# Kernel optimization log

Measured on AMD Instinct MI355X. Metric: run time of the kernel, lower is better.

Reference implementation:

```python
import jax, jax.numpy as jnp
import numpy as np

N_NODES = 50000
N_EDGES = 800000
D_IN = 128
D_GAT = 128
D_LIN = 512
D_OUT = 4
N_CONVS = 3


def setup_inputs() -> dict:
    key = jax.random.key(0)
    ks = jax.random.split(key, 16)
    s = 1.0 / np.sqrt(D_GAT)
    inp = {
        "x": jax.random.normal(ks[0], (N_NODES, D_IN), dtype=jnp.float32),
        "edge_index": jax.random.randint(ks[1], (2, N_EDGES), 0, N_NODES, dtype=jnp.int64),
        # 3 GATConv layers (input_dim == hidden_gat_dim so params stack)
        "conv_W": jax.random.normal(ks[2], (N_CONVS, D_GAT, D_GAT), dtype=jnp.float32) * s,
        "conv_a_src": jax.random.normal(ks[3], (N_CONVS, D_GAT), dtype=jnp.float32) * s,
        "conv_a_dst": jax.random.normal(ks[4], (N_CONVS, D_GAT), dtype=jnp.float32) * s,
        "conv_b": jnp.zeros((N_CONVS, D_GAT), dtype=jnp.float32),
        # MLP head: 128->512, 512->512, 512->512, 512->4
        "lin_W0": jax.random.normal(ks[5], (D_GAT, D_LIN), dtype=jnp.float32) / np.sqrt(D_GAT),
        "lin_b0": jnp.zeros((D_LIN,), dtype=jnp.float32),
        "lin_W1": jax.random.normal(ks[6], (D_LIN, D_LIN), dtype=jnp.float32) / np.sqrt(D_LIN),
        "lin_b1": jnp.zeros((D_LIN,), dtype=jnp.float32),
        "lin_W2": jax.random.normal(ks[7], (D_LIN, D_LIN), dtype=jnp.float32) / np.sqrt(D_LIN),
        "lin_b2": jnp.zeros((D_LIN,), dtype=jnp.float32),
        "lin_Wout": jax.random.normal(ks[8], (D_LIN, D_OUT), dtype=jnp.float32) / np.sqrt(D_LIN),
        "lin_bout": jnp.zeros((D_OUT,), dtype=jnp.float32),
    }
    return inp


def _gat_layer(x, src, dst, W, a_src, a_dst, b, n):
    """PyG-style single-head GATConv with self loops already in (src, dst)."""
    h = x @ W                                    # [N, F]
    e = (h @ a_src)[src] + (h @ a_dst)[dst]      # per-edge raw score [E]
    e = jax.nn.leaky_relu(e, 0.2)
    # segment softmax over destination node neighborhoods
    m = jax.ops.segment_max(e, dst, num_segments=n)
    ex = jnp.exp(e - m[dst])
    denom = jax.ops.segment_sum(ex, dst, num_segments=n)
    alpha = ex / denom[dst]                      # [E]
    out = jax.ops.segment_sum(alpha[:, None] * h[src], dst, num_segments=n)
    return out + b


def reference(x, edge_index, conv_W, conv_a_src, conv_a_dst, conv_b,
              lin_W0, lin_b0, lin_W1, lin_b1, lin_W2, lin_b2, lin_Wout, lin_bout):
    n = x.shape[0]
    loops = jnp.arange(n, dtype=edge_index.dtype)
    src = jnp.concatenate([edge_index[0], loops])  # add self loops (PyG default)
    dst = jnp.concatenate([edge_index[1], loops])
    for i in range(N_CONVS):
        x = _gat_layer(x, src, dst, conv_W[i], conv_a_src[i], conv_a_dst[i], conv_b[i], n)
        x = jax.nn.leaky_relu(x, 0.2)
    for W, b in ((lin_W0, lin_b0), (lin_W1, lin_b1), (lin_W2, lin_b2)):
        x = jax.nn.relu(x @ W + b)  # F.relu(x, 0.2): 0.2 is truthy inplace flag -> plain relu
    return x @ lin_Wout + lin_bout
```

## Files before the change

### kernel.cpp

```cpp
#include <hip/hip_runtime.h>
#include <hip/hip_bf16.h>

#define NN 50000
#define NE 800000
#define NET (NE + NN)
#define SCAN_NB ((NN + 255) / 256)

static inline int imin(int a, int b) { return a < b ? a : b; }

typedef _Float16 half8 __attribute__((ext_vector_type(8)));
typedef _Float16 half2v __attribute__((ext_vector_type(2)));
typedef float f32x4 __attribute__((ext_vector_type(4)));

__global__ void k_count(const int* __restrict__ edst, int* __restrict__ counts) {
    int e = blockIdx.x * blockDim.x + threadIdx.x;
    if (e >= NET) return;
    int d = (e < NE) ? edst[e] : (e - NE);
    atomicAdd(&counts[d], 1);
}

__global__ __launch_bounds__(256) void k_scan1(const int* __restrict__ counts,
                                               int* __restrict__ part) {
    __shared__ int s[256];
    int t = threadIdx.x, i = blockIdx.x * 256 + t;
    s[t] = (i < NN) ? counts[i] : 0;
    __syncthreads();
    for (int off = 128; off > 0; off >>= 1) {
        if (t < off) s[t] += s[t + off];
        __syncthreads();
    }
    if (t == 0) part[blockIdx.x] = s[0];
}

__global__ __launch_bounds__(256) void k_scan2(int* __restrict__ part, int* __restrict__ offs) {
    __shared__ int s[256];
    int t = threadIdx.x;
    int v = (t < SCAN_NB) ? part[t] : 0;
    s[t] = v;
    __syncthreads();
    for (int off = 1; off < 256; off <<= 1) {
        int a = (t >= off) ? s[t - off] : 0;
        __syncthreads();
        s[t] += a;
        __syncthreads();
    }
    if (t < SCAN_NB) part[t] = s[t] - v;
    if (t == 255) offs[NN] = s[255];
}

__global__ __launch_bounds__(256) void k_scan3(const int* __restrict__ counts,
                                               const int* __restrict__ part,
                                               int* __restrict__ offs, int* __restrict__ cursor) {
    __shared__ int s[256];
    int t = threadIdx.x, i = blockIdx.x * 256 + t;
    int v = (i < NN) ? counts[i] : 0;
    s[t] = v;
    __syncthreads();
    for (int off = 1; off < 256; off <<= 1) {
        int a = (t >= off) ? s[t - off] : 0;
        __syncthreads();
        s[t] += a;
        __syncthreads();
    }
    if (i < NN) {
        int e = part[blockIdx.x] + s[t] - v;
        offs[i] = e;
        cursor[i] = e;
    }
}

__global__ void k_scatter(const int* __restrict__ esrc, const int* __restrict__ edst,
                          int* __restrict__ cursor, int* __restrict__ csr_src) {
    int e = blockIdx.x * blockDim.x + threadIdx.x;
    if (e >= NET) return;
    int s, d;
    if (e < NE) { s = esrc[e]; d = edst[e]; } else { s = e - NE; d = s; }
    int pos = atomicAdd(&cursor[d], 1);
    csr_src[pos] = s;
}

__global__ void k_split(const float* __restrict__ in, _Float16* __restrict__ hi,
                        _Float16* __restrict__ lo, int n) {
    int i = blockIdx.x * blockDim.x + threadIdx.x;
    int st = gridDim.x * blockDim.x;
    for (; i < n; i += st) {
        float v = in[i];
        _Float16 h = (_Float16)v;
        hi[i] = h;
        lo[i] = (_Float16)(v - (float)h);
    }
}

__global__ __launch_bounds__(256) void k_prepw(const float* __restrict__ W,
                                               _Float16* __restrict__ Th,
                                               _Float16* __restrict__ Tl, int K, int N) {
    __shared__ float tile[32][33];
    int tx = threadIdx.x & 31, ty = threadIdx.x >> 5;
    int n0 = blockIdx.x * 32, k0 = blockIdx.y * 32;
    #pragma unroll
    for (int r = ty; r < 32; r += 8)
        tile[r][tx] = W[(size_t)(k0 + r) * N + n0 + tx];
    __syncthreads();
    #pragma unroll
    for (int r = ty; r < 32; r += 8) {
        int n = n0 + r, k = k0 + tx;
        float v = tile[tx][r];
        _Float16 h = (_Float16)v;
        Th[(size_t)n * K + k] = h;
        Tl[(size_t)n * K + k] = (_Float16)(v - (float)h);
    }
}

__global__ void k_aggregate(const _Float16* __restrict__ h, const float* __restrict__ s_src,
                            const float* __restrict__ s_dst, const int* __restrict__ offs,
                            const int* __restrict__ csr_src, const float* __restrict__ bias,
                            _Float16* __restrict__ xh, _Float16* __restrict__ xl) {
    int node = blockIdx.x * 4 + (threadIdx.x >> 6);
    int lane = threadIdx.x & 63;
    if (node >= NN) return;
    int p = offs[node], pe = offs[node + 1];
    float sd = s_dst[node];
    float den = 0.f, acc0 = 0.f, acc1 = 0.f;
    for (; p + 4 <= pe; p += 4) {
        int s0 = csr_src[p + 0], s1 = csr_src[p + 1];
        int s2 = csr_src[p + 2], s3 = csr_src[p + 3];
        float e0 = s_src[s0] + sd, e1 = s_src[s1] + sd;
        float e2 = s_src[s2] + sd, e3 = s_src[s3] + sd;
        half2v a0 = *((const half2v*)(h + (size_t)s0 * 128) + lane);
        half2v a1 = *((const half2v*)(h + (size_t)s1 * 128) + lane);
        half2v a2 = *((const half2v*)(h + (size_t)s2 * 128) + lane);
        half2v a3 = *((const half2v*)(h + (size_t)s3 * 128) + lane);
        e0 = (e0 > 0.f) ? e0 : 0.2f * e0;  float w0 = __expf(e0);
        e1 = (e1 > 0.f) ? e1 : 0.2f * e1;  float w1 = __expf(e1);
        e2 = (e2 > 0.f) ? e2 : 0.2f * e2;  float w2 = __expf(e2);
        e3 = (e3 > 0.f) ? e3 : 0.2f * e3;  float w3 = __expf(e3);
        den += (w0 + w1) + (w2 + w3);
        acc0 += w0 * (float)a0[0] + w1 * (float)a1[0] + w2 * (float)a2[0] + w3 * (float)a3[0];
        acc1 += w0 * (float)a0[1] + w1 * (float)a1[1] + w2 * (float)a2[1] + w3 * (float)a3[1];
    }
    for (; p < pe; ++p) {
        int src = csr_src[p];
        float e = s_src[src] + sd;
        e = (e > 0.f) ? e : 0.2f * e;
        float wgt = __expf(e);
        den += wgt;
        half2v av = *((const half2v*)(h + (size_t)src * 128) + lane);
        acc0 += wgt * (float)av[0];
        acc1 += wgt * (float)av[1];
    }
    float inv = 1.f / den;
    float2 bv = *((const float2*)bias + lane);
    float v0 = acc0 * inv + bv.x;
    float v1 = acc1 * inv + bv.y;
    v0 = (v0 > 0.f) ? v0 : 0.2f * v0;
    v1 = (v1 > 0.f) ? v1 : 0.2f * v1;
    _Float16 h0 = (_Float16)v0, h1 = (_Float16)v1;
    size_t base = (size_t)node * 128 + 2 * lane;
    *(half2v*)(xh + base) = (half2v){h0, h1};
    *(half2v*)(xl + base) = (half2v){(_Float16)(v0 - (float)h0), (_Float16)(v1 - (float)h1)};
}

__device__ __forceinline__ void gload_lds16(const void* g, void* l) {
    __builtin_amdgcn_global_load_lds(
        (const __attribute__((address_space(1))) void*)g,
        (__attribute__((address_space(3))) void*)l, 16, 0, 0);
}

__device__ __forceinline__ void phase_stagger(int bid) {
    int ph = (int)(((unsigned)bid * 2654435761u) >> 29);
    for (int i = 0; i < ph; ++i) __builtin_amdgcn_s_sleep(8);
}

__global__ __launch_bounds__(512) void k_mgemm(
    const _Float16* __restrict__ Ahi, const _Float16* __restrict__ Alo,
    const _Float16* __restrict__ Bhi, const _Float16* __restrict__ Blo,
    const float* __restrict__ bias, float* __restrict__ Cf,
    _Float16* __restrict__ Chi, _Float16* __restrict__ Clo,
    int M, int N, int K, int relu, int split, int nx, int ntiles)
{
    __shared__ _Float16 sm[4][128][32];

    int bid = blockIdx.x;
    int per = (ntiles + 7) >> 3;
    int g = (bid & 7) * per + (bid >> 3);
    if (g >= ntiles) return;
    int col0 = (g % nx) * 128;
    int row0 = (g / nx) * 128;

    phase_stagger(bid);

    int t = threadIdx.x;
    int w = t >> 6, lane = t & 63;
    int wm = (w & 3) * 32, wn = (w >> 2) * 64;
    int fr = lane & 15;
    int fq = lane >> 4, fq8 = fq * 8;

    int srow = t >> 2;
    int scol = (t & 3) << 3;
    int lrow = w << 4;

    f32x4 acc[2][4];
    #pragma unroll
    for (int i = 0; i < 2; i++)
        #pragma unroll
        for (int j = 0; j < 4; j++) acc[i][j] = (f32x4){0.f, 0.f, 0.f, 0.f};

    for (int k0 = 0; k0 < K; k0 += 32) {
        if (k0) __syncthreads();
        {
            int ga = row0 + srow; if (ga > M - 1) ga = M - 1;
            int gb = col0 + srow;
            gload_lds16(Ahi + (size_t)ga * K + k0 + scol, &sm[0][lrow][0]);
            gload_lds16(Alo + (size_t)ga * K + k0 + scol, &sm[1][lrow][0]);
            gload_lds16(Bhi + (size_t)gb * K + k0 + scol, &sm[2][lrow][0]);
            gload_lds16(Blo + (size_t)gb * K + k0 + scol, &sm[3][lrow][0]);
        }
        __syncthreads();

        half8 bh[4], bl[4];
        #pragma unroll
        for (int ni = 0; ni < 4; ++ni) {
            bh[ni] = *(half8*)&sm[2][wn + ni * 16 + fr][fq8];
            bl[ni] = *(half8*)&sm[3][wn + ni * 16 + fr][fq8];
        }
        #pragma unroll
        for (int mi = 0; mi < 2; ++mi) {
            half8 ah = *(half8*)&sm[0][wm + mi * 16 + fr][fq8];
            half8 al = *(half8*)&sm[1][wm + mi * 16 + fr][fq8];
            #pragma unroll
            for (int ni = 0; ni < 4; ++ni) {
                acc[mi][ni] = __builtin_amdgcn_mfma_f32_16x16x32_f16(ah, bh[ni], acc[mi][ni], 0, 0, 0);
                acc[mi][ni] = __builtin_amdgcn_mfma_f32_16x16x32_f16(ah, bl[ni], acc[mi][ni], 0, 0, 0);
                acc[mi][ni] = __builtin_amdgcn_mfma_f32_16x16x32_f16(al, bh[ni], acc[mi][ni], 0, 0, 0);
            }
        }
    }

    float bv[4];
    #pragma unroll
    for (int ni = 0; ni < 4; ++ni)
        bv[ni] = bias ? bias[col0 + wn + ni * 16 + fr] : 0.f;

    if (split) {
        _Float16* sc = &sm[0][0][0];
        #pragma unroll
        for (int pass = 0; pass < 2; ++pass) {
            __syncthreads();
            #pragma unroll
            for (int mi = 0; mi < 2; ++mi) {
                #pragma unroll
                for (int ni = 0; ni < 4; ++ni) {
                    #pragma unroll
                    for (int r = 0; r < 4; ++r) {
                        int row = wm + mi * 16 + fq * 4 + r;
                        int col = wn + ni * 16 + fr;
                        float v = acc[mi][ni][r] + bv[ni];
                        if (relu) v = (v > 0.f) ? v : 0.f;
                        _Float16 hh = (_Float16)v;
                        sc[row * 128 + col] = pass ? (_Float16)(v - (float)hh) : hh;
                    }
                }
            }
            __syncthreads();
            _Float16* dst = pass ? Clo : Chi;
            #pragma unroll
            for (int pp = 0; pp < 4; ++pp) {
                int idx = t + pp * 512;
                int row = idx >> 4, seg = idx & 15;
                int gr = row0 + row;
                if (gr < M)
                    *(half8*)(dst + (size_t)gr * N + col0 + seg * 8) =
                        *(half8*)&sc[row * 128 + seg * 8];
            }
        }
    } else {
        #pragma unroll
        for (int ni = 0; ni < 4; ++ni) {
            #pragma unroll
            for (int mi = 0; mi < 2; ++mi) {
                #pragma unroll
                for (int r = 0; r < 4; ++r) {
                    int gr = row0 + wm + mi * 16 + fq * 4 + r;
                    if (gr >= M) continue;
                    float v = acc[mi][ni][r] + bv[ni];
                    if (relu) v = (v > 0.f) ? v : 0.f;
                    Cf[(size_t)gr * N + col0 + wn + ni * 16 + fr] = v;
                }
            }
        }
    }
}

__global__ __launch_bounds__(256) void k_mgemm_gat(
    const _Float16* __restrict__ Ahi, const _Float16* __restrict__ Alo,
    const _Float16* __restrict__ Bhi, const _Float16* __restrict__ Blo,
    const float* __restrict__ a_src, const float* __restrict__ a_dst,
    _Float16* __restrict__ hbuf, float* __restrict__ s_src, float* __restrict__ s_dst,
    int M, int ntiles)
{
    __shared__ _Float16 sm[4][128][32];
    __shared__ float sps[2][128], spd[2][128];

    const int K = 128;
    int bid = blockIdx.x;
    int per = (ntiles + 7) >> 3;
    int g = (bid & 7) * per + (bid >> 3);
    if (g >= ntiles) return;
    int row0 = g * 128;

    int t = threadIdx.x;
    int w = t >> 6, lane = t & 63;
    int wm = (w & 1) * 64, wn = (w >> 1) * 64;
    int fr = lane & 15;
    int fq = lane >> 4, fq8 = fq * 8;
    int wnIdx = w >> 1;

    int srow = (w << 5) + (lane >> 2);
    int scol = (lane & 3) << 3;

    f32x4 acc[4][4];
    #pragma unroll
    for (int i = 0; i < 4; i++)
        #pragma unroll
        for (int j = 0; j < 4; j++) acc[i][j] = (f32x4){0.f, 0.f, 0.f, 0.f};

    for (int k0 = 0; k0 < K; k0 += 32) {
        if (k0) __syncthreads();
        #pragma unroll
        for (int i = 0; i < 2; ++i) {
            int rr = srow + i * 16;
            int ga = row0 + rr; if (ga > M - 1) ga = M - 1;
            int gb = rr;
            int lr = (w << 5) + i * 16;
            gload_lds16(Ahi + (size_t)ga * K + k0 + scol, &sm[0][lr][0]);
            gload_lds16(Alo + (size_t)ga * K + k0 + scol, &sm[1][lr][0]);
            gload_lds16(Bhi + (size_t)gb * K + k0 + scol, &sm[2][lr][0]);
            gload_lds16(Blo + (size_t)gb * K + k0 + scol, &sm[3][lr][0]);
        }
        __syncthreads();

        half8 bh[4], bl[4];
        #pragma unroll
        for (int ni = 0; ni < 4; ++ni) {
            bh[ni] = *(half8*)&sm[2][wn + ni * 16 + fr][fq8];
            bl[ni] = *(half8*)&sm[3][wn + ni * 16 + fr][fq8];
        }
        #pragma unroll
        for (int mi = 0; mi < 4; ++mi) {
            half8 ah = *(half8*)&sm[0][wm + mi * 16 + fr][fq8];
            half8 al = *(half8*)&sm[1][wm + mi * 16 + fr][fq8];
            #pragma unroll
            for (int ni = 0; ni < 4; ++ni) {
                acc[mi][ni] = __builtin_amdgcn_mfma_f32_16x16x32_f16(ah, bh[ni], acc[mi][ni], 0, 0, 0);
                acc[mi][ni] = __builtin_amdgcn_mfma_f32_16x16x32_f16(ah, bl[ni], acc[mi][ni], 0, 0, 0);
                acc[mi][ni] = __builtin_amdgcn_mfma_f32_16x16x32_f16(al, bh[ni], acc[mi][ni], 0, 0, 0);
            }
        }
    }

    float asv[4], adv[4];
    #pragma unroll
    for (int ni = 0; ni < 4; ++ni) {
        int gc = wn + ni * 16 + fr;
        asv[ni] = a_src[gc];
        adv[ni] = a_dst[gc];
    }
    #pragma unroll
    for (int mi = 0; mi < 4; ++mi) {
        #pragma unroll
        for (int r = 0; r < 4; ++r) {
            int lr = wm + mi * 16 + fq * 4 + r;
            int gr = row0 + lr;
            float vps = 0.f, vpd = 0.f;
            #pragma unroll
            for (int ni = 0; ni < 4; ++ni) {
                float v = acc[mi][ni][r];
                vps += v * asv[ni];
                vpd += v * adv[ni];
                if (gr < M) hbuf[(size_t)gr * 128 + wn + ni * 16 + fr] = (_Float16)v;
            }
            #pragma unroll
            for (int off = 1; off < 16; off <<= 1) {
                vps += __shfl_xor(vps, off);
                vpd += __shfl_xor(vpd, off);
            }
            if (fr == 0) { sps[wnIdx][lr] = vps; spd[wnIdx][lr] = vpd; }
        }
    }
    __syncthreads();
    if (t < 128) {
        int gr = row0 + t;
        if (gr < M) {
            s_src[gr] = sps[0][t] + sps[1][t];
            s_dst[gr] = spd[0][t] + spd[1][t];
        }
    }
}

__global__ __launch_bounds__(256) void k_mgemm_head(
    const _Float16* __restrict__ Ahi, const _Float16* __restrict__ Alo,
    const _Float16* __restrict__ Bhi, const _Float16* __restrict__ Blo,
    const float* __restrict__ bias, const float* __restrict__ Wo,
    float* __restrict__ partial,
    int M, int K, int nx, int ntiles)
{
    __shared__ _Float16 sm[4][128][32];
    __shared__ float4 sacc[2][128];

    int bid = blockIdx.x;
    int per = (ntiles + 7) >> 3;
    int g = (bid & 7) * per + (bid >> 3);
    if (g >= ntiles) return;
    int ct = g % nx;
    int col0 = ct * 128;
    int row0 = (g / nx) * 128;

    phase_stagger(bid);

    int t = threadIdx.x;
    int w = t >> 6, lane = t & 63;
    int wm = (w & 1) * 64, wn = (w >> 1) * 64;
    int fr = lane & 15;
    int fq = lane >> 4, fq8 = fq * 8;

    int srow = (w << 5) + (lane >> 2);
    int scol = (lane & 3) << 3;

    f32x4 acc[4][4];
    #pragma unroll
    for (int i = 0; i < 4; i++)
        #pragma unroll
        for (int j = 0; j < 4; j++) acc[i][j] = (f32x4){0.f, 0.f, 0.f, 0.f};

    for (int k0 = 0; k0 < K; k0 += 32) {
        if (k0) __syncthreads();
        #pragma unroll
        for (int i = 0; i < 2; ++i) {
            int rr = srow + i * 16;
            int ga = row0 + rr; if (ga > M - 1) ga = M - 1;
            int gb = col0 + rr;
            int lr = (w << 5) + i * 16;
            gload_lds16(Ahi + (size_t)ga * K + k0 + scol, &sm[0][lr][0]);
            gload_lds16(Alo + (size_t)ga * K + k0 + scol, &sm[1][lr][0]);
            gload_lds16(Bhi + (size_t)gb * K + k0 + scol, &sm[2][lr][0]);
            gload_lds16(Blo + (size_t)gb * K + k0 + scol, &sm[3][lr][0]);
        }
        __syncthreads();

        half8 bh[4], bl[4];
        #pragma unroll
        for (int ni = 0; ni < 4; ++ni) {
            bh[ni] = *(half8*)&sm[2][wn + ni * 16 + fr][fq8];
            bl[ni] = *(half8*)&sm[3][wn + ni * 16 + fr][fq8];
        }
        #pragma unroll
        for (int mi = 0; mi < 4; ++mi) {
            half8 ah = *(half8*)&sm[0][wm + mi * 16 + fr][fq8];
            half8 al = *(half8*)&sm[1][wm + mi * 16 + fr][fq8];
            #pragma unroll
            for (int ni = 0; ni < 4; ++ni) {
                acc[mi][ni] = __builtin_amdgcn_mfma_f32_16x16x32_f16(ah, bh[ni], acc[mi][ni], 0, 0, 0);
                acc[mi][ni] = __builtin_amdgcn_mfma_f32_16x16x32_f16(ah, bl[ni], acc[mi][ni], 0, 0, 0);
                acc[mi][ni] = __builtin_amdgcn_mfma_f32_16x16x32_f16(al, bh[ni], acc[mi][ni], 0, 0, 0);
            }
        }
    }

    float bv[4];
    float4 wv[4];
    #pragma unroll
    for (int ni = 0; ni < 4; ++ni) {
        int gc = col0 + wn + ni * 16 + fr;
        bv[ni] = bias[gc];
        wv[ni] = *(const float4*)(Wo + (size_t)gc * 4);
    }
    #pragma unroll
    for (int mi = 0; mi < 4; ++mi) {
        #pragma unroll
        for (int r = 0; r < 4; ++r) {
            int lr = wm + mi * 16 + fq * 4 + r;
            float o0 = 0.f, o1 = 0.f, o2 = 0.f, o3 = 0.f;
            #pragma unroll
            for (int ni = 0; ni < 4; ++ni) {
                float v = acc[mi][ni][r] + bv[ni];
                v = (v > 0.f) ? v : 0.f;
                o0 += v * wv[ni].x; o1 += v * wv[ni].y;
                o2 += v * wv[ni].z; o3 += v * wv[ni].w;
            }
            #pragma unroll
            for (int off = 1; off < 16; off <<= 1) {
                o0 += __shfl_xor(o0, off); o1 += __shfl_xor(o1, off);
                o2 += __shfl_xor(o2, off); o3 += __shfl_xor(o3, off);
            }
            if (fr == 0) sacc[w >> 1][lr] = (float4){o0, o1, o2, o3};
        }
    }
    __syncthreads();
    if (t < 128) {
        int gr = row0 + t;
        if (gr < M) {
            float4 s0 = sacc[0][t], s1 = sacc[1][t];
            float4 o = (float4){s0.x + s1.x, s0.y + s1.y, s0.z + s1.z, s0.w + s1.w};
            *(float4*)(partial + ((size_t)ct * M + gr) * 4) = o;
        }
    }
}

__global__ __launch_bounds__(256) void k_headred(const float* __restrict__ partial,
                                                 const float* __restrict__ bo,
                                                 float* __restrict__ out, int M) {
    int r = blockIdx.x * 256 + threadIdx.x;
    if (r >= M) return;
    float4 a = *(const float4*)(partial + ((size_t)0 * M + r) * 4);
    float4 b = *(const float4*)(partial + ((size_t)1 * M + r) * 4);
    float4 c = *(const float4*)(partial + ((size_t)2 * M + r) * 4);
    float4 d = *(const float4*)(partial + ((size_t)3 * M + r) * 4);
    float4 o;
    o.x = a.x + b.x + c.x + d.x + bo[0];
    o.y = a.y + b.y + c.y + d.y + bo[1];
    o.z = a.z + b.z + c.z + d.z + bo[2];
    o.w = a.w + b.w + c.w + d.w + bo[3];
    *(float4*)(out + (size_t)r * 4) = o;
}

extern "C" void kernel_launch(void* const* d_in, const int* in_sizes, int n_in,
                              void* d_out, int out_size, void* d_ws, size_t ws_size,
                              hipStream_t stream) {
    const float* x    = (const float*)d_in[0];
    const int*   eidx = (const int*)d_in[1];
    const float* cW   = (const float*)d_in[2];
    const float* caS  = (const float*)d_in[3];
    const float* caD  = (const float*)d_in[4];
    const float* cB   = (const float*)d_in[5];
    const float* W0   = (const float*)d_in[6];
    const float* b0   = (const float*)d_in[7];
    const float* W1   = (const float*)d_in[8];
    const float* b1   = (const float*)d_in[9];
    const float* W2   = (const float*)d_in[10];
    const float* b2   = (const float*)d_in[11];
    const float* Wo   = (const float*)d_in[12];
    const float* bo   = (const float*)d_in[13];
    (void)in_sizes; (void)n_in; (void)out_size;

    const int* esrc = eidx;
    const int* edst = eidx + NE;
    float* out = (float*)d_out;

    char* w = (char*)d_ws;
    auto alloc = [&](size_t bytes) -> char* {
        char* p = w;
        w += (bytes + 255) & ~(size_t)255;
        return p;
    };
    _Float16* x0h  = (_Float16*)alloc((size_t)NN * 128 * 2);
    _Float16* x0l  = (_Float16*)alloc((size_t)NN * 128 * 2);
    _Float16* xh   = (_Float16*)alloc((size_t)NN * 128 * 2);
    _Float16* xl   = (_Float16*)alloc((size_t)NN * 128 * 2);
    _Float16* hbuf = (_Float16*)alloc((size_t)NN * 128 * 2);
    float* ssrc    = (float*)alloc((size_t)NN * 4);
    float* sdst    = (float*)alloc((size_t)NN * 4);
    int*   counts  = (int*)  alloc((size_t)NN * 4);
    int*   offs    = (int*)  alloc((size_t)(NN + 1) * 4);
    int*   cursor  = (int*)  alloc((size_t)NN * 4);
    int*   csr     = (int*)  alloc((size_t)NET * 4);
    int*   part    = (int*)  alloc((size_t)SCAN_NB * 4);
    _Float16* cwh  = (_Float16*)alloc(3 * 128 * 128 * 2);
    _Float16* cwl  = (_Float16*)alloc(3 * 128 * 128 * 2);
    _Float16* w0h  = (_Float16*)alloc(512 * 128 * 2);
    _Float16* w0l  = (_Float16*)alloc(512 * 128 * 2);
    _Float16* w1h  = (_Float16*)alloc(512 * 512 * 2);
    _Float16* w1l  = (_Float16*)alloc(512 * 512 * 2);
    _Float16* w2h  = (_Float16*)alloc(512 * 512 * 2);
    _Float16* w2l  = (_Float16*)alloc(512 * 512 * 2);
    float* hpart   = (float*)alloc((size_t)4 * NN * 4 * 4);

    size_t used = (size_t)(w - (char*)d_ws);
    size_t rem = (ws_size > used) ? (ws_size - used) : 0;
    int chunk = (int)(rem / (4 * 512 * sizeof(_Float16)));
    if (chunk > NN) chunk = NN;
    if (chunk > 128) chunk &= ~127;
    if (chunk < 1) chunk = 1;
    _Float16* Y0h = (_Float16*)alloc((size_t)chunk * 512 * 2);
    _Float16* Y0l = (_Float16*)alloc((size_t)chunk * 512 * 2);
    _Float16* Y1h = (_Float16*)alloc((size_t)chunk * 512 * 2);
    _Float16* Y1l = (_Float16*)alloc((size_t)chunk * 512 * 2);

    auto gemm = [&](const _Float16* Ah, const _Float16* Al,
                    const _Float16* Bh, const _Float16* Bl,
                    const float* bias, float* Cf, _Float16* Ch, _Float16* Cl,
                    int M, int N, int K, int relu, int split) {
        int nx = N / 128;
        int ntiles = nx * ((M + 127) / 128);
        int nb = ((ntiles + 7) / 8) * 8;
        k_mgemm<<<nb, 512, 0, stream>>>(Ah, Al, Bh, Bl, bias, Cf, Ch, Cl,
                                        M, N, K, relu, split, nx, ntiles);
    };

    k_split<<<2048, 256, 0, stream>>>(x, x0h, x0l, NN * 128);
    for (int L = 0; L < 3; ++L)
        k_prepw<<<dim3(128 / 32, 128 / 32), 256, 0, stream>>>(
            cW + (size_t)L * 128 * 128, cwh + (size_t)L * 128 * 128, cwl + (size_t)L * 128 * 128, 128, 128);
    k_prepw<<<dim3(512 / 32, 128 / 32), 256, 0, stream>>>(W0, w0h, w0l, 128, 512);
    k_prepw<<<dim3(512 / 32, 512 / 32), 256, 0, stream>>>(W1, w1h, w1l, 512, 512);
    k_prepw<<<dim3(512 / 32, 512 / 32), 256, 0, stream>>>(W2, w2h, w2l, 512, 512);

    hipMemsetAsync(counts, 0, (size_t)NN * 4, stream);
    int eblocks = (NET + 255) / 256;
    k_count <<<eblocks, 256, 0, stream>>>(edst, counts);
    k_scan1 <<<SCAN_NB, 256, 0, stream>>>(counts, part);
    k_scan2 <<<1, 256, 0, stream>>>(part, offs);
    k_scan3 <<<SCAN_NB, 256, 0, stream>>>(counts, part, offs, cursor);
    k_scatter<<<eblocks, 256, 0, stream>>>(esrc, edst, cursor, csr);

    int gat_tiles = (NN + 127) / 128;
    int gat_nb = ((gat_tiles + 7) / 8) * 8;
    for (int L = 0; L < 3; ++L) {
        const _Float16* Ah = (L == 0) ? x0h : xh;
        const _Float16* Al = (L == 0) ? x0l : xl;
        k_mgemm_gat<<<gat_nb, 256, 0, stream>>>(
            Ah, Al, cwh + (size_t)L * 128 * 128, cwl + (size_t)L * 128 * 128,
            caS + L * 128, caD + L * 128, hbuf, ssrc, sdst, NN, gat_tiles);
        k_aggregate<<<NN / 4, 256, 0, stream>>>(hbuf, ssrc, sdst, offs, csr, cB + L * 128, xh, xl);
    }

    for (int m0 = 0; m0 < NN; m0 += chunk) {
        int cm = imin(chunk, NN - m0);
        gemm(xh + (size_t)m0 * 128, xl + (size_t)m0 * 128, w0h, w0l, b0,
             nullptr, Y0h, Y0l, cm, 512, 128, 1, 1);
        gemm(Y0h, Y0l, w1h, w1l, b1, nullptr, Y1h, Y1l, cm, 512, 512, 1, 1);
        int nx = 4;
        int ntiles = nx * ((cm + 127) / 128);
        int nb = ((ntiles + 7) / 8) * 8;
        k_mgemm_head<<<nb, 256, 0, stream>>>(Y1h, Y1l, w2h, w2l, b2, Wo,
                                             hpart, cm, 512, nx, ntiles);
        k_headred<<<(cm + 255) / 256, 256, 0, stream>>>(hpart, bo, out + (size_t)m0 * 4, cm);
    }
}
```

Measured before the change: 649.6 us.

## Use 512-thread blocks with 8 waves in GAT and head GEMMs, stage hbuf via LDS

Doubles the block size of the GAT projection and head GEMM kernels from 4 to 8 waves. Each wave now computes a 32x64 sub-tile instead of 64x64, which halves the accumulator registers per wave and means each thread issues one set of global-to-LDS loads per K step instead of two. The GAT kernel also writes its fp16 output tile to shared memory first and then copies it to global memory with coalesced 16-byte row stores. The trade-off is more waves sharing the same tile with less MFMA work each, and one extra barrier plus an LDS round trip in the epilogue.

```diff
diff --git a/kernel.cpp b/kernel.cpp
--- a/kernel.cpp
+++ b/kernel.cpp
@@ -291,7 +291,7 @@
     }
 }
 
-__global__ __launch_bounds__(256) void k_mgemm_gat(
+__global__ __launch_bounds__(512) void k_mgemm_gat(
     const _Float16* __restrict__ Ahi, const _Float16* __restrict__ Alo,
     const _Float16* __restrict__ Bhi, const _Float16* __restrict__ Blo,
     const float* __restrict__ a_src, const float* __restrict__ a_dst,
@@ -310,32 +310,30 @@
 
     int t = threadIdx.x;
     int w = t >> 6, lane = t & 63;
-    int wm = (w & 1) * 64, wn = (w >> 1) * 64;
+    int wm = (w & 3) * 32, wn = (w >> 2) * 64;
     int fr = lane & 15;
     int fq = lane >> 4, fq8 = fq * 8;
-    int wnIdx = w >> 1;
-
-    int srow = (w << 5) + (lane >> 2);
-    int scol = (lane & 3) << 3;
-
-    f32x4 acc[4][4];
-    #pragma unroll
-    for (int i = 0; i < 4; i++)
+    int wnIdx = w >> 2;
+
+    int srow = t >> 2;
+    int scol = (t & 3) << 3;
+    int lrow = w << 4;
+
+    f32x4 acc[2][4];
+    #pragma unroll
+    for (int i = 0; i < 2; i++)
         #pragma unroll
         for (int j = 0; j < 4; j++) acc[i][j] = (f32x4){0.f, 0.f, 0.f, 0.f};
 
     for (int k0 = 0; k0 < K; k0 += 32) {
         if (k0) __syncthreads();
-        #pragma unroll
-        for (int i = 0; i < 2; ++i) {
-            int rr = srow + i * 16;
-            int ga = row0 + rr; if (ga > M - 1) ga = M - 1;
-            int gb = rr;
-            int lr = (w << 5) + i * 16;
-            gload_lds16(Ahi + (size_t)ga * K + k0 + scol, &sm[0][lr][0]);
-            gload_lds16(Alo + (size_t)ga * K + k0 + scol, &sm[1][lr][0]);
-            gload_lds16(Bhi + (size_t)gb * K + k0 + scol, &sm[2][lr][0]);
-            gload_lds16(Blo + (size_t)gb * K + k0 + scol, &sm[3][lr][0]);
+        {
+            int ga = row0 + srow; if (ga > M - 1) ga = M - 1;
+            int gb = srow;
+            gload_lds16(Ahi + (size_t)ga * K + k0 + scol, &sm[0][lrow][0]);
+            gload_lds16(Alo + (size_t)ga * K + k0 + scol, &sm[1][lrow][0]);
+            gload_lds16(Bhi + (size_t)gb * K + k0 + scol, &sm[2][lrow][0]);
+            gload_lds16(Blo + (size_t)gb * K + k0 + scol, &sm[3][lrow][0]);
         }
         __syncthreads();
 
@@ -346,7 +344,7 @@
             bl[ni] = *(half8*)&sm[3][wn + ni * 16 + fr][fq8];
         }
         #pragma unroll
-        for (int mi = 0; mi < 4; ++mi) {
+        for (int mi = 0; mi < 2; ++mi) {
             half8 ah = *(half8*)&sm[0][wm + mi * 16 + fr][fq8];
             half8 al = *(half8*)&sm[1][wm + mi * 16 + fr][fq8];
             #pragma unroll
@@ -365,26 +363,27 @@
         asv[ni] = a_src[gc];
         adv[ni] = a_dst[gc];
     }
-    #pragma unroll
-    for (int mi = 0; mi < 4; ++mi) {
+    __syncthreads();
+    _Float16* sc = &sm[0][0][0];
+    #pragma unroll
+    for (int mi = 0; mi < 2; ++mi) {
         #pragma unroll
         for (int r = 0; r < 4; ++r) {
-            int lr = wm + mi * 16 + fq * 4 + r;
-            int gr = row0 + lr;
+            int row = wm + mi * 16 + fq * 4 + r;
             float vps = 0.f, vpd = 0.f;
             #pragma unroll
             for (int ni = 0; ni < 4; ++ni) {
                 float v = acc[mi][ni][r];
                 vps += v * asv[ni];
                 vpd += v * adv[ni];
-                if (gr < M) hbuf[(size_t)gr * 128 + wn + ni * 16 + fr] = (_Float16)v;
+                sc[row * 128 + wn + ni * 16 + fr] = (_Float16)v;
             }
             #pragma unroll
             for (int off = 1; off < 16; off <<= 1) {
                 vps += __shfl_xor(vps, off);
                 vpd += __shfl_xor(vpd, off);
             }
-            if (fr == 0) { sps[wnIdx][lr] = vps; spd[wnIdx][lr] = vpd; }
+            if (fr == 0) { sps[wnIdx][row] = vps; spd[wnIdx][row] = vpd; }
         }
     }
     __syncthreads();
@@ -395,9 +394,17 @@
             s_dst[gr] = spd[0][t] + spd[1][t];
         }
     }
-}
-
-__global__ __launch_bounds__(256) void k_mgemm_head(
+    #pragma unroll
+    for (int pp = 0; pp < 4; ++pp) {
+        int idx = t + pp * 512;
+        int row = idx >> 4, seg = idx & 15;
+        int gr = row0 + row;
+        if (gr < M)
+            *(half8*)(hbuf + (size_t)gr * 128 + seg * 8) = *(half8*)&sc[row * 128 + seg * 8];
+    }
+}
+
+__global__ __launch_bounds__(512) void k_mgemm_head(
     const _Float16* __restrict__ Ahi, const _Float16* __restrict__ Alo,
     const _Float16* __restrict__ Bhi, const _Float16* __restrict__ Blo,
     const float* __restrict__ bias, const float* __restrict__ Wo,
@@ -419,31 +426,29 @@
 
     int t = threadIdx.x;
     int w = t >> 6, lane = t & 63;
-    int wm = (w & 1) * 64, wn = (w >> 1) * 64;
+    int wm = (w & 3) * 32, wn = (w >> 2) * 64;
     int fr = lane & 15;
     int fq = lane >> 4, fq8 = fq * 8;
 
-    int srow = (w << 5) + (lane >> 2);
-    int scol = (lane & 3) << 3;
-
-    f32x4 acc[4][4];
-    #pragma unroll
-    for (int i = 0; i < 4; i++)
+    int srow = t >> 2;
+    int scol = (t & 3) << 3;
+    int lrow = w << 4;
+
+    f32x4 acc[2][4];
+    #pragma unroll
+    for (int i = 0; i < 2; i++)
         #pragma unroll
         for (int j = 0; j < 4; j++) acc[i][j] = (f32x4){0.f, 0.f, 0.f, 0.f};
 
     for (int k0 = 0; k0 < K; k0 += 32) {
         if (k0) __syncthreads();
-        #pragma unroll
-        for (int i = 0; i < 2; ++i) {
-            int rr = srow + i * 16;
-            int ga = row0 + rr; if (ga > M - 1) ga = M - 1;
-            int gb = col0 + rr;
-            int lr = (w << 5) + i * 16;
-            gload_lds16(Ahi + (size_t)ga * K + k0 + scol, &sm[0][lr][0]);
-            gload_lds16(Alo + (size_t)ga * K + k0 + scol, &sm[1][lr][0]);
-            gload_lds16(Bhi + (size_t)gb * K + k0 + scol, &sm[2][lr][0]);
-            gload_lds16(Blo + (size_t)gb * K + k0 + scol, &sm[3][lr][0]);
+        {
+            int ga = row0 + srow; if (ga > M - 1) ga = M - 1;
+            int gb = col0 + srow;
+            gload_lds16(Ahi + (size_t)ga * K + k0 + scol, &sm[0][lrow][0]);
+            gload_lds16(Alo + (size_t)ga * K + k0 + scol, &sm[1][lrow][0]);
+            gload_lds16(Bhi + (size_t)gb * K + k0 + scol, &sm[2][lrow][0]);
+            gload_lds16(Blo + (size_t)gb * K + k0 + scol, &sm[3][lrow][0]);
         }
         __syncthreads();
 
@@ -454,7 +459,7 @@
             bl[ni] = *(half8*)&sm[3][wn + ni * 16 + fr][fq8];
         }
         #pragma unroll
-        for (int mi = 0; mi < 4; ++mi) {
+        for (int mi = 0; mi < 2; ++mi) {
             half8 ah = *(half8*)&sm[0][wm + mi * 16 + fr][fq8];
             half8 al = *(half8*)&sm[1][wm + mi * 16 + fr][fq8];
             #pragma unroll
@@ -475,10 +480,10 @@
         wv[ni] = *(const float4*)(Wo + (size_t)gc * 4);
     }
     #pragma unroll
-    for (int mi = 0; mi < 4; ++mi) {
+    for (int mi = 0; mi < 2; ++mi) {
         #pragma unroll
         for (int r = 0; r < 4; ++r) {
-            int lr = wm + mi * 16 + fq * 4 + r;
+            int row = wm + mi * 16 + fq * 4 + r;
             float o0 = 0.f, o1 = 0.f, o2 = 0.f, o3 = 0.f;
             #pragma unroll
             for (int ni = 0; ni < 4; ++ni) {
@@ -492,7 +497,7 @@
                 o0 += __shfl_xor(o0, off); o1 += __shfl_xor(o1, off);
                 o2 += __shfl_xor(o2, off); o3 += __shfl_xor(o3, off);
             }
-            if (fr == 0) sacc[w >> 1][lr] = (float4){o0, o1, o2, o3};
+            if (fr == 0) sacc[w >> 2][row] = (float4){o0, o1, o2, o3};
         }
     }
     __syncthreads();
@@ -617,7 +622,7 @@
     for (int L = 0; L < 3; ++L) {
         const _Float16* Ah = (L == 0) ? x0h : xh;
         const _Float16* Al = (L == 0) ? x0l : xl;
-        k_mgemm_gat<<<gat_nb, 256, 0, stream>>>(
+        k_mgemm_gat<<<gat_nb, 512, 0, stream>>>(
             Ah, Al, cwh + (size_t)L * 128 * 128, cwl + (size_t)L * 128 * 128,
             caS + L * 128, caD + L * 128, hbuf, ssrc, sdst, NN, gat_tiles);
         k_aggregate<<<NN / 4, 256, 0, stream>>>(hbuf, ssrc, sdst, offs, csr, cB + L * 128, xh, xl);
@@ -631,7 +636,7 @@
         int nx = 4;
         int ntiles = nx * ((cm + 127) / 128);
         int nb = ((ntiles + 7) / 8) * 8;
-        k_mgemm_head<<<nb, 256, 0, stream>>>(Y1h, Y1l, w2h, w2l, b2, Wo,
+        k_mgemm_head<<<nb, 512, 0, stream>>>(Y1h, Y1l, w2h, w2l, b2, Wo,
                                              hpart, cm, 512, nx, ntiles);
         k_headred<<<(cm + 255) / 256, 256, 0, stream>>>(hpart, bo, out + (size_t)m0 * 4, cm);
     }
```

New measurement: 653.6 us. Within noise of the previous version (+0.6%).
